# Performance work log

Hardware: AMD Instinct MI355X
Metric: run time of the kernel (lower is better)

Reference implementation:

```python
import jax, jax.numpy as jnp
import numpy as np

NUM_HEADS = 16

def setup_inputs() -> dict:
    key = jax.random.key(0)
    ks = jax.random.split(key, 6)
    B, S, D = 4, 2048, 1024
    sc = 1.0 / np.sqrt(D)
    return {
        "x": jax.random.normal(ks[0], (B, S, D), jnp.float32),
        "Wq": jax.random.normal(ks[1], (D, D), jnp.float32) * sc,
        "Wk": jax.random.normal(ks[2], (D, D), jnp.float32) * sc,
        "Wv": jax.random.normal(ks[3], (D, D), jnp.float32) * sc,
        "Wo": jax.random.normal(ks[4], (D, D), jnp.float32) * sc,
        "bo": jnp.zeros((D,), jnp.float32),
    }

def reference(x, Wq, Wk, Wv, Wo, bo):
    B, S, D = x.shape
    H = NUM_HEADS
    hd = D // H
    # projections (Linear: x @ W^T, but we store W as [d_in, d_out] so x @ W)
    q = (x @ Wq).reshape(B, S, H, hd)
    k = (x @ Wk).reshape(B, S, H, hd)
    v = (x @ Wv).reshape(B, S, H, hd)
    # scores: [B, H, S, S]
    scores = jnp.einsum("bqhd,bkhd->bhqk", q, k) / jnp.sqrt(jnp.asarray(hd, x.dtype))
    attn = jax.nn.softmax(scores, axis=-1)  # dropout p=0.0 (eval) -> identity
    ctx = jnp.einsum("bhqk,bkhd->bqhd", attn, v).reshape(B, S, D)
    return ctx @ Wo + bo
```

## Files before the change

kernel.cpp:

```cpp
#include <hip/hip_runtime.h>
#include <hip/hip_bf16.h>

typedef __bf16 bf16x8 __attribute__((ext_vector_type(8)));
typedef float f32x4 __attribute__((ext_vector_type(4)));

#define D_MODEL 1024
#define SEQ 2048
#define BATCH 4
#define HEADS 16
#define HD 64
#define M_TOT (BATCH * SEQ)
#define QPW 4

static __device__ __forceinline__ unsigned short f2bf(float f) {
  unsigned int u = __float_as_uint(f);
  unsigned int lsb = (u >> 16) & 1u;
  u += 0x7fffu + lsb;
  return (unsigned short)(u >> 16);
}

__global__ __launch_bounds__(256) void cvt_x_kernel(const float* __restrict__ x,
                                                    unsigned short* __restrict__ xb,
                                                    int n4) {
  int i = blockIdx.x * 256 + threadIdx.x;
  if (i >= n4) return;
  const float4 v = reinterpret_cast<const float4*>(x)[i];
  ushort4 o;
  o.x = f2bf(v.x); o.y = f2bf(v.y); o.z = f2bf(v.z); o.w = f2bf(v.w);
  reinterpret_cast<ushort4*>(xb)[i] = o;
}

__global__ __launch_bounds__(256) void transW4_kernel(
    const float* __restrict__ Wq, const float* __restrict__ Wk,
    const float* __restrict__ Wv, const float* __restrict__ Wo,
    unsigned short* __restrict__ WqT, unsigned short* __restrict__ WkT,
    unsigned short* __restrict__ WvT, unsigned short* __restrict__ WoT) {
  const float* W;
  unsigned short* Wt;
  switch (blockIdx.z) {
    case 0: W = Wq; Wt = WqT; break;
    case 1: W = Wk; Wt = WkT; break;
    case 2: W = Wv; Wt = WvT; break;
    default: W = Wo; Wt = WoT; break;
  }
  __shared__ float t[32][33];
  int bx = blockIdx.x * 32;
  int by = blockIdx.y * 32;
  int tx = threadIdx.x, ty = threadIdx.y;
#pragma unroll
  for (int i = 0; i < 32; i += 8)
    t[ty + i][tx] = W[(size_t)(by + ty + i) * D_MODEL + bx + tx];
  __syncthreads();
#pragma unroll
  for (int i = 0; i < 32; i += 8)
    Wt[(size_t)(bx + ty + i) * D_MODEL + by + tx] = f2bf(t[tx][ty + i]);
}

__global__ __launch_bounds__(256) void gemm_qkv_kernel(
    const unsigned short* __restrict__ A, const unsigned short* __restrict__ WqT,
    const unsigned short* __restrict__ WkT, const unsigned short* __restrict__ WvT,
    unsigned short* __restrict__ Qb, unsigned short* __restrict__ Kb,
    unsigned short* __restrict__ Vb, float qscale) {
  __shared__ __align__(16) unsigned short Als[128][72];
  __shared__ __align__(16) unsigned short Bls[128][72];

  const int tid = threadIdx.x;
  const int l = tid & 63;
  const int wave = tid >> 6;
  const int l15 = l & 15;
  const int lk = l >> 4;
  const int wm = wave >> 1, wn = wave & 1;

  const int bid = blockIdx.x;
  const int nid = (bid & 7) * 192 + (bid >> 3);
  const int mblk = nid / 24;
  const int rem = nid % 24;
  const int which = rem >> 3;
  const int nblk = rem & 7;
  const int m0 = mblk << 7, n0 = nblk << 7;

  const unsigned short* Bt = which == 0 ? WqT : (which == 1 ? WkT : WvT);
  const float scale = which == 0 ? qscale : 1.0f;

  f32x4 acc[4][4] = {};

  const int srow = tid >> 3;
  const int scol = (tid & 7) * 8;

  bf16x8 areg[4], breg[4];
#pragma unroll
  for (int i = 0; i < 4; ++i) {
    areg[i] = *reinterpret_cast<const bf16x8*>(&A[(size_t)(m0 + srow + i * 32) * D_MODEL + scol]);
    breg[i] = *reinterpret_cast<const bf16x8*>(&Bt[(size_t)(n0 + srow + i * 32) * D_MODEL + scol]);
  }

  for (int k0 = 0; k0 < D_MODEL; k0 += 64) {
    __syncthreads();
#pragma unroll
    for (int i = 0; i < 4; ++i) {
      *reinterpret_cast<bf16x8*>(&Als[srow + i * 32][scol]) = areg[i];
      *reinterpret_cast<bf16x8*>(&Bls[srow + i * 32][scol]) = breg[i];
    }
    __syncthreads();

    if (k0 + 64 < D_MODEL) {
#pragma unroll
      for (int i = 0; i < 4; ++i) {
        areg[i] = *reinterpret_cast<const bf16x8*>(
            &A[(size_t)(m0 + srow + i * 32) * D_MODEL + k0 + 64 + scol]);
        breg[i] = *reinterpret_cast<const bf16x8*>(
            &Bt[(size_t)(n0 + srow + i * 32) * D_MODEL + k0 + 64 + scol]);
      }
    }

#pragma unroll
    for (int kk = 0; kk < 2; ++kk) {
      bf16x8 af[4], bfr[4];
#pragma unroll
      for (int m = 0; m < 4; ++m)
        af[m] = *reinterpret_cast<const bf16x8*>(&Als[wm * 64 + m * 16 + l15][kk * 32 + lk * 8]);
#pragma unroll
      for (int n = 0; n < 4; ++n)
        bfr[n] = *reinterpret_cast<const bf16x8*>(&Bls[wn * 64 + n * 16 + l15][kk * 32 + lk * 8]);
#pragma unroll
      for (int m = 0; m < 4; ++m)
#pragma unroll
        for (int n = 0; n < 4; ++n)
          acc[m][n] = __builtin_amdgcn_mfma_f32_16x16x32_bf16(af[m], bfr[n], acc[m][n], 0, 0, 0);
    }
  }

  unsigned short* out = which == 0 ? Qb : (which == 1 ? Kb : Vb);
#pragma unroll
  for (int m = 0; m < 4; ++m) {
#pragma unroll
    for (int n = 0; n < 4; ++n) {
      const int row0 = wm * 64 + m * 16 + lk * 4;
      const int col = wn * 64 + n * 16 + l15;
      const int gm0 = m0 + row0;
      const int gn = n0 + col;
      if (which < 2) {
#pragma unroll
        for (int r = 0; r < 4; ++r)
          out[(size_t)(gm0 + r) * D_MODEL + gn] = f2bf(acc[m][n][r] * scale);
      } else {
        int b = gm0 >> 11, s = gm0 & 2047;
        int h = gn >> 6, d = gn & 63;
        size_t base = ((size_t)((b * HEADS + h) * HD + d)) * SEQ + s;
#pragma unroll
        for (int r = 0; r < 4; ++r) out[base + r] = f2bf(acc[m][n][r]);
      }
    }
  }
}

__global__ __launch_bounds__(256) void gemm_out_kernel(
    const unsigned short* __restrict__ A, const unsigned short* __restrict__ Bt,
    float* __restrict__ out, const float* __restrict__ bias) {
  __shared__ __align__(16) unsigned short Als[128][72];
  __shared__ __align__(16) unsigned short Bls[128][72];

  const int tid = threadIdx.x;
  const int l = tid & 63;
  const int wave = tid >> 6;
  const int l15 = l & 15;
  const int lk = l >> 4;
  const int wm = wave >> 1, wn = wave & 1;

  const int nblocks_n = D_MODEL >> 7;
  const int mblk = blockIdx.x / nblocks_n;
  const int nblk = blockIdx.x % nblocks_n;
  const int m0 = mblk << 7, n0 = nblk << 7;

  f32x4 acc[4][4] = {};

  const int srow = tid >> 3;
  const int scol = (tid & 7) * 8;

  bf16x8 areg[4], breg[4];
#pragma unroll
  for (int i = 0; i < 4; ++i) {
    areg[i] = *reinterpret_cast<const bf16x8*>(&A[(size_t)(m0 + srow + i * 32) * D_MODEL + scol]);
    breg[i] = *reinterpret_cast<const bf16x8*>(&Bt[(size_t)(n0 + srow + i * 32) * D_MODEL + scol]);
  }

  for (int k0 = 0; k0 < D_MODEL; k0 += 64) {
    __syncthreads();
#pragma unroll
    for (int i = 0; i < 4; ++i) {
      *reinterpret_cast<bf16x8*>(&Als[srow + i * 32][scol]) = areg[i];
      *reinterpret_cast<bf16x8*>(&Bls[srow + i * 32][scol]) = breg[i];
    }
    __syncthreads();

    if (k0 + 64 < D_MODEL) {
#pragma unroll
      for (int i = 0; i < 4; ++i) {
        areg[i] = *reinterpret_cast<const bf16x8*>(
            &A[(size_t)(m0 + srow + i * 32) * D_MODEL + k0 + 64 + scol]);
        breg[i] = *reinterpret_cast<const bf16x8*>(
            &Bt[(size_t)(n0 + srow + i * 32) * D_MODEL + k0 + 64 + scol]);
      }
    }

#pragma unroll
    for (int kk = 0; kk < 2; ++kk) {
      bf16x8 af[4], bfr[4];
#pragma unroll
      for (int m = 0; m < 4; ++m)
        af[m] = *reinterpret_cast<const bf16x8*>(&Als[wm * 64 + m * 16 + l15][kk * 32 + lk * 8]);
#pragma unroll
      for (int n = 0; n < 4; ++n)
        bfr[n] = *reinterpret_cast<const bf16x8*>(&Bls[wn * 64 + n * 16 + l15][kk * 32 + lk * 8]);
#pragma unroll
      for (int m = 0; m < 4; ++m)
#pragma unroll
        for (int n = 0; n < 4; ++n)
          acc[m][n] = __builtin_amdgcn_mfma_f32_16x16x32_bf16(af[m], bfr[n], acc[m][n], 0, 0, 0);
    }
  }

#pragma unroll
  for (int m = 0; m < 4; ++m) {
#pragma unroll
    for (int n = 0; n < 4; ++n) {
      const int gm0 = m0 + wm * 64 + m * 16 + lk * 4;
      const int gn = n0 + wn * 64 + n * 16 + l15;
      const float bv = bias[gn];
#pragma unroll
      for (int r = 0; r < 4; ++r)
        out[(size_t)(gm0 + r) * D_MODEL + gn] = acc[m][n][r] + bv;
    }
  }
}

__global__ __launch_bounds__(256) void attn_kernel(const unsigned short* __restrict__ Q,
                                                   const unsigned short* __restrict__ Kb,
                                                   const unsigned short* __restrict__ Vt,
                                                   unsigned short* __restrict__ ctx) {
  __shared__ __align__(16) unsigned short Kls[2][64 * 64];
  __shared__ __align__(16) unsigned short Vls[2][64 * 64];

  const int tid = threadIdx.x;
  const int l = tid & 63;
  const int wave = tid >> 6;
  const int l15 = l & 15;
  const int lk = l >> 4;

  const int bid = blockIdx.x;
  const int nid = (bid & 7) * 64 + (bid >> 3);
  const int qt = nid & 7;
  const int bh = nid >> 3;
  const int b = bh >> 4;
  const int h = bh & 15;

  const int qbase = b * SEQ + qt * 256 + wave * 64;

  bf16x8 qf[QPW][2];
#pragma unroll
  for (int qb = 0; qb < QPW; ++qb)
#pragma unroll
    for (int kk = 0; kk < 2; ++kk)
      qf[qb][kk] = *reinterpret_cast<const bf16x8*>(
          &Q[(size_t)(qbase + qb * 16 + l15) * D_MODEL + h * HD + kk * 32 + lk * 8]);

  f32x4 acc[QPW][4] = {};
  float lsum[QPW] = {};

  const int srow = tid >> 2;
  const int sc = tid & 3;
  const int krow = (srow & 32) | ((srow & 4) << 2) | ((srow >> 1) & 12) | (srow & 3);

  const size_t kgbase = ((size_t)b * SEQ) * D_MODEL + h * HD;
  const size_t vgbase = ((size_t)(b * HEADS + h) * HD) * SEQ;

  uint4 kreg[2], vreg[2];
#pragma unroll
  for (int i = 0; i < 2; ++i) {
    kreg[i] = *reinterpret_cast<const uint4*>(
        &Kb[kgbase + (size_t)srow * D_MODEL + sc * 8 + i * 32]);
    vreg[i] = *reinterpret_cast<const uint4*>(
        &Vt[vgbase + (size_t)srow * SEQ + sc * 8 + i * 32]);
  }

  int p = 0;
  for (int kt = 0; kt < SEQ / 64; ++kt) {
    char* klsb = (char*)Kls[p];
    char* vlsb = (char*)Vls[p];
#pragma unroll
    for (int i = 0; i < 2; ++i) {
      *reinterpret_cast<uint4*>(
          klsb + krow * 128 + ((sc * 16 + i * 64) ^ ((krow & 7) << 4))) = kreg[i];
      *reinterpret_cast<uint4*>(
          vlsb + srow * 128 + ((sc * 16 + i * 64) ^ ((srow & 7) << 4))) = vreg[i];
    }
    __syncthreads();

    if (kt + 1 < SEQ / 64) {
      const int nt = kt + 1;
#pragma unroll
      for (int i = 0; i < 2; ++i) {
        kreg[i] = *reinterpret_cast<const uint4*>(
            &Kb[kgbase + (size_t)(nt * 64 + srow) * D_MODEL + sc * 8 + i * 32]);
        vreg[i] = *reinterpret_cast<const uint4*>(
            &Vt[vgbase + (size_t)srow * SEQ + nt * 64 + sc * 8 + i * 32]);
      }
    }

    f32x4 s[QPW][4] = {};
#pragma unroll
    for (int kk = 0; kk < 2; ++kk) {
      bf16x8 kf[4];
#pragma unroll
      for (int n = 0; n < 4; ++n)
        kf[n] = *reinterpret_cast<const bf16x8*>(
            klsb + (n * 16 + l15) * 128 + ((kk * 64 + lk * 16) ^ ((l15 & 7) << 4)));
#pragma unroll
      for (int qb = 0; qb < QPW; ++qb)
#pragma unroll
        for (int n = 0; n < 4; ++n)
          s[qb][n] = __builtin_amdgcn_mfma_f32_16x16x32_bf16(kf[n], qf[qb][kk], s[qb][n], 0, 0, 0);
    }

    bf16x8 pvv[QPW][2];
#pragma unroll
    for (int qb = 0; qb < QPW; ++qb) {
      float ps = 0.f;
#pragma unroll
      for (int n = 0; n < 4; ++n)
#pragma unroll
        for (int r = 0; r < 4; ++r) {
          float pp = __builtin_amdgcn_exp2f(s[qb][n][r]);
          ps += pp;
          pvv[qb][n >> 1][(n & 1) * 4 + r] = (__bf16)pp;
        }
      lsum[qb] += ps;
    }

#pragma unroll
    for (int kk = 0; kk < 2; ++kk) {
      bf16x8 vf[4];
#pragma unroll
      for (int nd = 0; nd < 4; ++nd)
        vf[nd] = *reinterpret_cast<const bf16x8*>(
            vlsb + (nd * 16 + l15) * 128 + ((kk * 64 + lk * 16) ^ ((l15 & 7) << 4)));
#pragma unroll
      for (int qb = 0; qb < QPW; ++qb)
#pragma unroll
        for (int nd = 0; nd < 4; ++nd)
          acc[qb][nd] = __builtin_amdgcn_mfma_f32_16x16x32_bf16(vf[nd], pvv[qb][kk], acc[qb][nd], 0, 0, 0);
    }
    p ^= 1;
  }

#pragma unroll
  for (int qb = 0; qb < QPW; ++qb) {
    float t = lsum[qb];
    t += __shfl_xor(t, 16);
    t += __shfl_xor(t, 32);
    const float inv = 1.0f / t;
    const size_t row = (size_t)(qbase + qb * 16 + l15) * D_MODEL + h * HD;
#pragma unroll
    for (int nd = 0; nd < 4; ++nd) {
      ushort4 ov;
      ov.x = f2bf(acc[qb][nd][0] * inv);
      ov.y = f2bf(acc[qb][nd][1] * inv);
      ov.z = f2bf(acc[qb][nd][2] * inv);
      ov.w = f2bf(acc[qb][nd][3] * inv);
      *reinterpret_cast<ushort4*>(&ctx[row + nd * 16 + lk * 4]) = ov;
    }
  }
}

extern "C" void kernel_launch(void* const* d_in, const int* in_sizes, int n_in,
                              void* d_out, int out_size, void* d_ws, size_t ws_size,
                              hipStream_t stream) {
  const float* x = (const float*)d_in[0];
  const float* Wq = (const float*)d_in[1];
  const float* Wk = (const float*)d_in[2];
  const float* Wv = (const float*)d_in[3];
  const float* Wo = (const float*)d_in[4];
  const float* bo = (const float*)d_in[5];

  char* ws = (char*)d_ws;
  const size_t MB = 1u << 20;
  unsigned short* xb = (unsigned short*)(ws + 0 * MB);
  unsigned short* WqT = (unsigned short*)(ws + 16 * MB);
  unsigned short* WkT = (unsigned short*)(ws + 18 * MB);
  unsigned short* WvT = (unsigned short*)(ws + 20 * MB);
  unsigned short* WoT = (unsigned short*)(ws + 22 * MB);
  unsigned short* Qb = (unsigned short*)(ws + 24 * MB);
  unsigned short* Kb = (unsigned short*)(ws + 40 * MB);
  unsigned short* Vt = (unsigned short*)(ws + 56 * MB);
  unsigned short* ctx = (unsigned short*)(ws + 72 * MB);

  int n4 = (M_TOT * D_MODEL) / 4;
  cvt_x_kernel<<<n4 / 256, 256, 0, stream>>>(x, xb, n4);

  transW4_kernel<<<dim3(32, 32, 4), dim3(32, 8), 0, stream>>>(Wq, Wk, Wv, Wo, WqT, WkT, WvT, WoT);

  gemm_qkv_kernel<<<3 * (M_TOT / 128) * (D_MODEL / 128), 256, 0, stream>>>(
      xb, WqT, WkT, WvT, Qb, Kb, Vt, 0.125f * 1.44269504f);

  attn_kernel<<<BATCH * HEADS * (SEQ / 256), 256, 0, stream>>>(Qb, Kb, Vt, ctx);

  gemm_out_kernel<<<(M_TOT / 128) * (D_MODEL / 128), 256, 0, stream>>>(ctx, WoT, (float*)d_out, bo);
}
```

Measured before the change: 219.6 us.

## Split attention over two key halves with a separate combine kernel

The attention grid is doubled so each block handles half of the key sequence. Each half writes its normalised bf16 output and its row sums to scratch buffers that reuse dead workspace (the xb and WqT regions). A new combine kernel blends the two partial outputs, weighted by their sums, into the context buffer. The goal is more blocks per CU to fill the GPU better. The costs are an extra kernel launch, extra global memory traffic, an extra bf16 rounding step, and removal of the register prefetch and double-buffered LDS pipeline in the key loop.

```diff
diff --git a/kernel.cpp b/kernel.cpp
--- a/kernel.cpp
+++ b/kernel.cpp
@@ -237,9 +237,12 @@
 __global__ __launch_bounds__(256) void attn_kernel(const unsigned short* __restrict__ Q,
                                                    const unsigned short* __restrict__ Kb,
                                                    const unsigned short* __restrict__ Vt,
-                                                   unsigned short* __restrict__ ctx) {
-  __shared__ __align__(16) unsigned short Kls[2][64 * 64];
-  __shared__ __align__(16) unsigned short Vls[2][64 * 64];
+                                                   unsigned short* __restrict__ o0,
+                                                   unsigned short* __restrict__ o1,
+                                                   float* __restrict__ l0,
+                                                   float* __restrict__ l1) {
+  __shared__ __align__(16) unsigned short Kls[64 * 64];
+  __shared__ __align__(16) unsigned short Vls[64 * 64];
 
   const int tid = threadIdx.x;
   const int l = tid & 63;
@@ -248,13 +251,15 @@
   const int lk = l >> 4;
 
   const int bid = blockIdx.x;
-  const int nid = (bid & 7) * 64 + (bid >> 3);
-  const int qt = nid & 7;
-  const int bh = nid >> 3;
+  const int nid = (bid & 7) * 128 + (bid >> 3);
+  const int ks = nid & 1;
+  const int qt = (nid >> 1) & 7;
+  const int bh = nid >> 4;
   const int b = bh >> 4;
   const int h = bh & 15;
 
   const int qbase = b * SEQ + qt * 256 + wave * 64;
+  const int kt0 = ks * 16;
 
   bf16x8 qf[QPW][2];
 #pragma unroll
@@ -274,38 +279,25 @@
   const size_t kgbase = ((size_t)b * SEQ) * D_MODEL + h * HD;
   const size_t vgbase = ((size_t)(b * HEADS + h) * HD) * SEQ;
 
-  uint4 kreg[2], vreg[2];
-#pragma unroll
-  for (int i = 0; i < 2; ++i) {
-    kreg[i] = *reinterpret_cast<const uint4*>(
-        &Kb[kgbase + (size_t)srow * D_MODEL + sc * 8 + i * 32]);
-    vreg[i] = *reinterpret_cast<const uint4*>(
-        &Vt[vgbase + (size_t)srow * SEQ + sc * 8 + i * 32]);
-  }
-
-  int p = 0;
-  for (int kt = 0; kt < SEQ / 64; ++kt) {
-    char* klsb = (char*)Kls[p];
-    char* vlsb = (char*)Vls[p];
-#pragma unroll
-    for (int i = 0; i < 2; ++i) {
-      *reinterpret_cast<uint4*>(
-          klsb + krow * 128 + ((sc * 16 + i * 64) ^ ((krow & 7) << 4))) = kreg[i];
-      *reinterpret_cast<uint4*>(
-          vlsb + srow * 128 + ((sc * 16 + i * 64) ^ ((srow & 7) << 4))) = vreg[i];
-    }
-    __syncthreads();
-
-    if (kt + 1 < SEQ / 64) {
-      const int nt = kt + 1;
+  char* klsb = (char*)Kls;
+  char* vlsb = (char*)Vls;
+
+  for (int kt = kt0; kt < kt0 + 16; ++kt) {
+    __syncthreads();
+    {
 #pragma unroll
       for (int i = 0; i < 2; ++i) {
-        kreg[i] = *reinterpret_cast<const uint4*>(
-            &Kb[kgbase + (size_t)(nt * 64 + srow) * D_MODEL + sc * 8 + i * 32]);
-        vreg[i] = *reinterpret_cast<const uint4*>(
-            &Vt[vgbase + (size_t)srow * SEQ + nt * 64 + sc * 8 + i * 32]);
+        uint4 kv = *reinterpret_cast<const uint4*>(
+            &Kb[kgbase + (size_t)(kt * 64 + srow) * D_MODEL + sc * 8 + i * 32]);
+        uint4 vv = *reinterpret_cast<const uint4*>(
+            &Vt[vgbase + (size_t)srow * SEQ + kt * 64 + sc * 8 + i * 32]);
+        *reinterpret_cast<uint4*>(
+            klsb + krow * 128 + ((sc * 16 + i * 64) ^ ((krow & 7) << 4))) = kv;
+        *reinterpret_cast<uint4*>(
+            vlsb + srow * 128 + ((sc * 16 + i * 64) ^ ((srow & 7) << 4))) = vv;
       }
     }
+    __syncthreads();
 
     f32x4 s[QPW][4] = {};
 #pragma unroll
@@ -350,16 +342,18 @@
         for (int nd = 0; nd < 4; ++nd)
           acc[qb][nd] = __builtin_amdgcn_mfma_f32_16x16x32_bf16(vf[nd], pvv[qb][kk], acc[qb][nd], 0, 0, 0);
     }
-    p ^= 1;
-  }
-
+  }
+
+  unsigned short* op = ks ? o1 : o0;
+  float* lp = ks ? l1 : l0;
 #pragma unroll
   for (int qb = 0; qb < QPW; ++qb) {
     float t = lsum[qb];
     t += __shfl_xor(t, 16);
     t += __shfl_xor(t, 32);
     const float inv = 1.0f / t;
-    const size_t row = (size_t)(qbase + qb * 16 + l15) * D_MODEL + h * HD;
+    const int grow = qbase + qb * 16 + l15;
+    const size_t row = (size_t)grow * D_MODEL + h * HD;
 #pragma unroll
     for (int nd = 0; nd < 4; ++nd) {
       ushort4 ov;
@@ -367,9 +361,42 @@
       ov.y = f2bf(acc[qb][nd][1] * inv);
       ov.z = f2bf(acc[qb][nd][2] * inv);
       ov.w = f2bf(acc[qb][nd][3] * inv);
-      *reinterpret_cast<ushort4*>(&ctx[row + nd * 16 + lk * 4]) = ov;
-    }
-  }
+      *reinterpret_cast<ushort4*>(&op[row + nd * 16 + lk * 4]) = ov;
+    }
+    if (l < 16) lp[grow * HEADS + h] = t;
+  }
+}
+
+static __device__ __forceinline__ unsigned int comb2(unsigned int u0, unsigned int u1,
+                                                     float w0, float w1) {
+  float a0 = __uint_as_float((u0 & 0xffffu) << 16);
+  float b0 = __uint_as_float(u0 & 0xffff0000u);
+  float a1 = __uint_as_float((u1 & 0xffffu) << 16);
+  float b1 = __uint_as_float(u1 & 0xffff0000u);
+  unsigned int lo = f2bf(a0 * w0 + a1 * w1);
+  unsigned int hi = f2bf(b0 * w0 + b1 * w1);
+  return lo | (hi << 16);
+}
+
+__global__ __launch_bounds__(256) void combine_kernel(unsigned short* __restrict__ o0,
+                                                      const unsigned short* __restrict__ o1,
+                                                      const float* __restrict__ l0,
+                                                      const float* __restrict__ l1) {
+  const int i = blockIdx.x * 256 + threadIdx.x;
+  const int row = i >> 7;
+  const int h = (i & 127) >> 3;
+  const float a = l0[row * HEADS + h];
+  const float b = l1[row * HEADS + h];
+  const float inv = 1.0f / (a + b);
+  const float w0 = a * inv, w1 = b * inv;
+  const uint4 x0 = reinterpret_cast<const uint4*>(o0)[i];
+  const uint4 x1 = reinterpret_cast<const uint4*>(o1)[i];
+  uint4 y;
+  y.x = comb2(x0.x, x1.x, w0, w1);
+  y.y = comb2(x0.y, x1.y, w0, w1);
+  y.z = comb2(x0.z, x1.z, w0, w1);
+  y.w = comb2(x0.w, x1.w, w0, w1);
+  reinterpret_cast<uint4*>(o0)[i] = y;
 }
 
 extern "C" void kernel_launch(void* const* d_in, const int* in_sizes, int n_in,
@@ -393,6 +420,8 @@
   unsigned short* Kb = (unsigned short*)(ws + 40 * MB);
   unsigned short* Vt = (unsigned short*)(ws + 56 * MB);
   unsigned short* ctx = (unsigned short*)(ws + 72 * MB);
+  float* l0 = (float*)(ws + 16 * MB);
+  float* l1 = (float*)(ws + 16 * MB + 512 * 1024);
 
   int n4 = (M_TOT * D_MODEL) / 4;
   cvt_x_kernel<<<n4 / 256, 256, 0, stream>>>(x, xb, n4);
@@ -402,7 +431,8 @@
   gemm_qkv_kernel<<<3 * (M_TOT / 128) * (D_MODEL / 128), 256, 0, stream>>>(
       xb, WqT, WkT, WvT, Qb, Kb, Vt, 0.125f * 1.44269504f);
 
-  attn_kernel<<<BATCH * HEADS * (SEQ / 256), 256, 0, stream>>>(Qb, Kb, Vt, ctx);
+  attn_kernel<<<BATCH * HEADS * (SEQ / 256) * 2, 256, 0, stream>>>(Qb, Kb, Vt, ctx, xb, l0, l1);
+  combine_kernel<<<(M_TOT * D_MODEL / 8) / 256, 256, 0, stream>>>(ctx, xb, l0, l1);
 
   gemm_out_kernel<<<(M_TOT / 128) * (D_MODEL / 128), 256, 0, stream>>>(ctx, WoT, (float*)d_out, bo);
 }
```

Measured after the change: 200.3 us (median of 2 runs). 8.8% less time.
